# Optimization experiments

Measured on AMD Instinct MI355X. Metric: run time of the kernel, lower is better.

## Reference

```python
import jax, jax.numpy as jnp
import numpy as np
from jax import lax

EPS = 1e-7
N_CLASS = 10
ROUTINGS = 3
DIM_PRIMARY = 8
DIM_DIGIT = 16


def squash(s, axis=-1):
    sq = jnp.sum(jnp.square(s), axis=axis, keepdims=True)
    scale = sq / (1.0 + sq) / jnp.sqrt(sq + EPS)
    return scale * s


def setup_inputs() -> dict:
    key = jax.random.key(0)
    ks = jax.random.split(key, 6)
    B, H, W, C = 16, 100, 64, 1
    x = jax.random.normal(ks[0], (B, H, W, C), dtype=jnp.float32)
    # conv1: 9x9, 1 -> 256, stride 1, valid, relu
    conv1_w = jax.random.normal(ks[1], (9, 9, 1, 256), dtype=jnp.float32) * 0.05
    conv1_b = jnp.zeros((256,), dtype=jnp.float32)
    # PrimaryCap conv: 9x9, 256 -> 32*8=256, stride 2, valid, linear
    pc_w = jax.random.normal(ks[2], (9, 9, 256, 256), dtype=jnp.float32) * 0.02
    pc_b = jnp.zeros((256,), dtype=jnp.float32)
    # primary caps: conv1 out 92x56 -> pc conv out 42x24 -> 42*24*32 = 32256 caps
    n_in_caps = 42 * 24 * 32
    caps_W = jax.random.normal(ks[3], (N_CLASS, n_in_caps, DIM_DIGIT, DIM_PRIMARY), dtype=jnp.float32) * 0.05
    return {"x": x, "conv1_w": conv1_w, "conv1_b": conv1_b, "pc_w": pc_w, "pc_b": pc_b, "caps_W": caps_W}


def reference(x, conv1_w, conv1_b, pc_w, pc_b, caps_W):
    dn = ("NHWC", "HWIO", "NHWC")
    # Conv1 + relu: [B,92,56,256]
    y = lax.conv_general_dilated(x, conv1_w, (1, 1), "VALID", dimension_numbers=dn) + conv1_b
    y = jax.nn.relu(y)
    # PrimaryCap conv (stride 2): [B,42,24,256]
    p = lax.conv_general_dilated(y, pc_w, (2, 2), "VALID", dimension_numbers=dn) + pc_b
    B = p.shape[0]
    # reshape to capsules [B, I, 8] and squash
    u = squash(p.reshape(B, -1, DIM_PRIMARY))
    # predictions u_hat[b,j,i,d] = W[j,i,d,k] u[b,i,k]  -> [B, J, I, 16]
    u_hat = jnp.einsum("bik,jidk->bjid", u, caps_W)
    # dynamic routing
    b = jnp.zeros(u_hat.shape[:3], dtype=u_hat.dtype)  # [B, J, I]
    v = None
    for r in range(ROUTINGS):
        c = jax.nn.softmax(b, axis=1)  # over output capsules J
        s = jnp.einsum("bji,bjid->bjd", c, u_hat)
        v = squash(s)  # [B, J, 16]
        if r < ROUTINGS - 1:
            b = b + jnp.einsum("bjd,bjid->bji", v, u_hat)
    return v
```

## Files before the change

kernel.cpp:

```cpp
#include <hip/hip_runtime.h>
#include <hip/hip_bf16.h>
#include <hip/hip_fp16.h>
#include <stdint.h>

typedef __bf16 bf16x8_t __attribute__((ext_vector_type(8)));
typedef float  f32x4_t  __attribute__((ext_vector_type(4)));

#define PLANE_H (16L * 32256 * 32)
#define PSTRIDE 4128768L

__device__ __forceinline__ void gld_lds16(const void* g, void* l) {
    __builtin_amdgcn_global_load_lds(
        (const __attribute__((address_space(1))) uint32_t*)g,
        (__attribute__((address_space(3))) uint32_t*)l, 16, 0, 0);
}

__global__ __launch_bounds__(256) void k_conv1(
    const float* __restrict__ x, const float* __restrict__ w,
    const float* __restrict__ bias, __hip_bfloat16* __restrict__ y)
{
    const int b  = blockIdx.x / 92;
    const int oh = blockIdx.x % 92;
    const int oc = threadIdx.x;
    float wr[81];
#pragma unroll
    for (int t = 0; t < 81; ++t) wr[t] = w[t * 256 + oc];
    const float bs = bias[oc];
    const float* xb = x + (b * 100 + oh) * 64;
    __hip_bfloat16* yb = y + ((b * 92 + oh) * 56) * 256 + oc;
    for (int owg = 0; owg < 56; owg += 4) {
        float a0 = bs, a1 = bs, a2 = bs, a3 = bs;
#pragma unroll
        for (int kh = 0; kh < 9; ++kh) {
            const float* xr = xb + kh * 64 + owg;
            float xv[12];
#pragma unroll
            for (int t = 0; t < 12; ++t) xv[t] = xr[t];
#pragma unroll
            for (int kw = 0; kw < 9; ++kw) {
                const float wv = wr[kh * 9 + kw];
                a0 = fmaf(xv[kw + 0], wv, a0);
                a1 = fmaf(xv[kw + 1], wv, a1);
                a2 = fmaf(xv[kw + 2], wv, a2);
                a3 = fmaf(xv[kw + 3], wv, a3);
            }
        }
        yb[(owg + 0) * 256] = __float2bfloat16(fmaxf(a0, 0.f));
        yb[(owg + 1) * 256] = __float2bfloat16(fmaxf(a1, 0.f));
        yb[(owg + 2) * 256] = __float2bfloat16(fmaxf(a2, 0.f));
        yb[(owg + 3) * 256] = __float2bfloat16(fmaxf(a3, 0.f));
    }
}

__global__ __launch_bounds__(256) void k_wt(
    const float* __restrict__ w, __hip_bfloat16* __restrict__ wt)
{
    const int idx = blockIdx.x * 256 + threadIdx.x;
    const int oc  = idx / 20736;
    const int k   = idx - oc * 20736;
    wt[idx] = __float2bfloat16(w[k * 256 + oc]);
}

__global__ __launch_bounds__(256, 2) void k_pcconv2(
    const __hip_bfloat16* __restrict__ y,
    const __hip_bfloat16* __restrict__ wt,
    float* __restrict__ pbase)
{
    __shared__ __hip_bfloat16 lA[128 * 32];
    __shared__ __hip_bfloat16 lB[256 * 32];
    const int mbx = (blockIdx.x & 7) * 16 + (blockIdx.x >> 3);
    if (mbx >= 126) return;
    const int z = blockIdx.y;
    float* __restrict__ p = pbase + (long)z * PSTRIDE;

    const int tid  = threadIdx.x;
    const int trow = tid >> 2;
    const int quad = tid & 3;
    const int sq   = quad ^ ((trow >> 1) & 3);

    int ybase[2];
#pragma unroll
    for (int r = 0; r < 2; ++r) {
        const int m  = mbx * 128 + r * 64 + trow;
        const int b  = m / 1008;
        const int rm = m - b * 1008;
        const int oh = rm / 24;
        const int ow = rm - oh * 24;
        ybase[r] = ((b * 92 + 2 * oh) * 56 + 2 * ow) * 256 + sq * 8;
    }
    int wbase[4];
#pragma unroll
    for (int r = 0; r < 4; ++r)
        wbase[r] = (r * 64 + trow) * 20736 + sq * 8;

    f32x4_t acc[4][8];
#pragma unroll
    for (int mi = 0; mi < 4; ++mi)
#pragma unroll
        for (int ni = 0; ni < 8; ++ni)
            acc[mi][ni] = (f32x4_t){0.f, 0.f, 0.f, 0.f};

    const int wv   = tid >> 6;
    const int lane = tid & 63;
    const int mw   = (wv >> 1) * 64;
    const int nwb  = (wv & 1) * 128;
    const int lr   = lane & 15;
    const int lq   = lane >> 4;
    const int koff = (lq ^ ((lr >> 1) & 3)) * 8;

    for (int kc = z * 108; kc < z * 108 + 108; ++kc) {
        const int k0   = kc * 32;
        const int khw  = k0 >> 8;
        const int ic0  = k0 & 255;
        const int kh   = khw / 9;
        const int kw2  = khw - kh * 9;
        const int aoff = (kh * 56 + kw2) * 256 + ic0;
        __syncthreads();
#pragma unroll
        for (int r = 0; r < 2; ++r)
            gld_lds16(y + ybase[r] + aoff, &lA[r * 2048 + tid * 8]);
#pragma unroll
        for (int r = 0; r < 4; ++r)
            gld_lds16(wt + wbase[r] + k0, &lB[r * 2048 + tid * 8]);
        __builtin_amdgcn_s_waitcnt(0);
        __syncthreads();
        bf16x8_t af[4], bfr[8];
#pragma unroll
        for (int mi = 0; mi < 4; ++mi)
            af[mi] = *(const bf16x8_t*)&lA[(mw + mi * 16 + lr) * 32 + koff];
#pragma unroll
        for (int ni = 0; ni < 8; ++ni)
            bfr[ni] = *(const bf16x8_t*)&lB[(nwb + ni * 16 + lr) * 32 + koff];
#pragma unroll
        for (int mi = 0; mi < 4; ++mi)
#pragma unroll
            for (int ni = 0; ni < 8; ++ni)
                acc[mi][ni] = __builtin_amdgcn_mfma_f32_16x16x32_bf16(
                    af[mi], bfr[ni], acc[mi][ni], 0, 0, 0);
    }
#pragma unroll
    for (int mi = 0; mi < 4; ++mi)
#pragma unroll
        for (int ni = 0; ni < 8; ++ni) {
            const int col = nwb + ni * 16 + lr;
#pragma unroll
            for (int rr = 0; rr < 4; ++rr) {
                const int row = mbx * 128 + mw + mi * 16 + lq * 4 + rr;
                p[row * 256 + col] = acc[mi][ni][rr];
            }
        }
}

__global__ __launch_bounds__(256) void k_squash(
    const float* __restrict__ P, const float* __restrict__ bias, float* u)
{
    const int g = blockIdx.x * 256 + threadIdx.x;
    const int base = g * 8;
    const int cb = (g & 31) * 8;
    float v[8];
#pragma unroll
    for (int t = 0; t < 8; ++t) v[t] = bias[cb + t];
#pragma unroll
    for (int z = 0; z < 6; ++z) {
        const float4 a0 = *(const float4*)(P + z * PSTRIDE + base);
        const float4 a1 = *(const float4*)(P + z * PSTRIDE + base + 4);
        v[0] += a0.x; v[1] += a0.y; v[2] += a0.z; v[3] += a0.w;
        v[4] += a1.x; v[5] += a1.y; v[6] += a1.z; v[7] += a1.w;
    }
    float sq = 0.f;
#pragma unroll
    for (int t = 0; t < 8; ++t) sq += v[t] * v[t];
    const float sc = sq / ((1.f + sq) * sqrtf(sq + 1e-7f));
#pragma unroll
    for (int t = 0; t < 8; ++t) u[base + t] = v[t] * sc;
}

__global__ __launch_bounds__(256) void k_uhat2(
    const float* __restrict__ u, const float* __restrict__ W, __half* __restrict__ uh)
{
    __shared__ __half lbuf[8 * 64 * 32];
    const int bh  = blockIdx.x;
    const int ic  = blockIdx.y;
    const int tid = threadIdx.x;
    const int q   = tid & 3;
    const int il  = tid >> 2;
    const int i   = ic * 64 + il;

    for (int jg = 0; jg < 5; ++jg) {
        const float* wb0 = W + ((long)(2 * jg) * 32256 + i) * 128 + q * 32;
        const float* wb1 = wb0 + (long)32256 * 128;
        float4 w0[8], w1[8];
#pragma unroll
        for (int t = 0; t < 8; ++t) w0[t] = *(const float4*)(wb0 + t * 4);
#pragma unroll
        for (int t = 0; t < 8; ++t) w1[t] = *(const float4*)(wb1 + t * 4);
        if (jg) __syncthreads();
#pragma unroll
        for (int b = 0; b < 8; ++b) {
            const float* up = u + ((bh * 8 + b) * 32256 + i) * 8;
            const float4 u0 = *(const float4*)up;
            const float4 u1 = *(const float4*)(up + 4);
            union { __half h[8]; uint4 v; } pk;
#pragma unroll
            for (int d = 0; d < 4; ++d) {
                const float4 a = w0[2 * d], c = w0[2 * d + 1];
                pk.h[d] = __float2half(
                    a.x * u0.x + a.y * u0.y + a.z * u0.z + a.w * u0.w +
                    c.x * u1.x + c.y * u1.y + c.z * u1.z + c.w * u1.w);
            }
#pragma unroll
            for (int d = 0; d < 4; ++d) {
                const float4 a = w1[2 * d], c = w1[2 * d + 1];
                pk.h[4 + d] = __float2half(
                    a.x * u0.x + a.y * u0.y + a.z * u0.z + a.w * u0.w +
                    c.x * u1.x + c.y * u1.y + c.z * u1.z + c.w * u1.w);
            }
            *(uint4*)&lbuf[(b * 64 + il) * 32 + q * 8] = pk.v;
        }
        __syncthreads();
        __half* pb = uh + (long)jg * PLANE_H + ((long)(bh * 8) * 32256 + ic * 64) * 32;
#pragma unroll
        for (int b = 0; b < 8; ++b) {
            const uint4 v = *(const uint4*)&lbuf[b * 2048 + tid * 8];
            *(uint4*)(pb + (long)b * (32256 * 32) + tid * 8) = v;
        }
    }
}

__global__ __launch_bounds__(256) void k_route4(
    const __half* __restrict__ uh, const float* __restrict__ vsum,
    float* __restrict__ sp)
{
    __shared__ float red[4 * 160];
    const int b     = blockIdx.x;
    const int chunk = blockIdx.y;
    const int tid   = threadIdx.x;
    const int lane  = tid & 63;
    const int wv    = tid >> 6;
    const int q     = lane & 3;
    const int ig    = lane >> 2;

    float vs[10][4];
#pragma unroll
    for (int j = 0; j < 10; ++j) {
        const float4 t = *(const float4*)(vsum + (b * 10 + j) * 16 + q * 4);
        vs[j][0] = t.x; vs[j][1] = t.y; vs[j][2] = t.z; vs[j][3] = t.w;
    }
    float acc[10][4];
#pragma unroll
    for (int j = 0; j < 10; ++j)
#pragma unroll
        for (int t = 0; t < 4; ++t) acc[j][t] = 0.f;

    const int ib = chunk * 576 + wv * 16 + ig;
    for (int ps = 0; ps < 9; ++ps) {
        const int i = ib + ps * 64;
        const long rb = ((long)b * 32256 + i) * 32 + q * 8;
        uint4 r[5];
#pragma unroll
        for (int jg = 0; jg < 5; ++jg)
            r[jg] = *(const uint4*)(uh + jg * PLANE_H + rb);
        float uhf[10][4];
#pragma unroll
        for (int jg = 0; jg < 5; ++jg) {
            const unsigned wd[4] = {r[jg].x, r[jg].y, r[jg].z, r[jg].w};
#pragma unroll
            for (int h2 = 0; h2 < 4; ++h2) {
                const __half2 hh = *(const __half2*)&wd[h2];
                const int j  = jg * 2 + (h2 >> 1);
                const int d0 = (h2 & 1) * 2;
                uhf[j][d0 + 0] = __low2float(hh);
                uhf[j][d0 + 1] = __high2float(hh);
            }
        }
        float logit[10];
#pragma unroll
        for (int j = 0; j < 10; ++j) {
            float lg = vs[j][0] * uhf[j][0] + vs[j][1] * uhf[j][1]
                     + vs[j][2] * uhf[j][2] + vs[j][3] * uhf[j][3];
            lg += __shfl_xor(lg, 1);
            lg += __shfl_xor(lg, 2);
            logit[j] = lg;
        }
        float mx = logit[0];
#pragma unroll
        for (int j = 1; j < 10; ++j) mx = fmaxf(mx, logit[j]);
        float den = 0.f, e[10];
#pragma unroll
        for (int j = 0; j < 10; ++j) { e[j] = __expf(logit[j] - mx); den += e[j]; }
        const float inv = __builtin_amdgcn_rcpf(den);
#pragma unroll
        for (int j = 0; j < 10; ++j) {
            const float c = e[j] * inv;
#pragma unroll
            for (int t = 0; t < 4; ++t) acc[j][t] = fmaf(c, uhf[j][t], acc[j][t]);
        }
    }
#pragma unroll
    for (int j = 0; j < 10; ++j)
#pragma unroll
        for (int t = 0; t < 4; ++t) {
            float v2 = acc[j][t];
            v2 += __shfl_xor(v2, 4);
            v2 += __shfl_xor(v2, 8);
            v2 += __shfl_xor(v2, 16);
            v2 += __shfl_xor(v2, 32);
            if (lane < 4) red[wv * 160 + j * 16 + q * 4 + t] = v2;
        }
    __syncthreads();
    if (tid < 160) {
        const float s = red[tid] + red[160 + tid] + red[320 + tid] + red[480 + tid];
        atomicAdd(&sp[b * 160 + tid], s);
    }
}

__global__ void k_finish(const float* __restrict__ sp, float* __restrict__ vsum,
                         float* __restrict__ out, const int fin)
{
    const int t = threadIdx.x;
    if (t >= 160) return;
    const float* s = sp + t * 16;
    float sv[16]; float sq = 0.f;
#pragma unroll
    for (int d = 0; d < 16; ++d) { sv[d] = s[d]; sq += sv[d] * sv[d]; }
    const float sc = sq / ((1.f + sq) * sqrtf(sq + 1e-7f));
    if (fin) {
#pragma unroll
        for (int d = 0; d < 16; ++d) out[t * 16 + d] = sv[d] * sc;
    } else {
        float* vp = vsum + t * 16;
#pragma unroll
        for (int d = 0; d < 16; ++d) vp[d] += sv[d] * sc;
    }
}

extern "C" void kernel_launch(void* const* d_in, const int* in_sizes, int n_in,
                              void* d_out, int out_size, void* d_ws, size_t ws_size,
                              hipStream_t stream)
{
    const float* x   = (const float*)d_in[0];
    const float* c1w = (const float*)d_in[1];
    const float* c1b = (const float*)d_in[2];
    const float* pcw = (const float*)d_in[3];
    const float* pcb = (const float*)d_in[4];
    const float* cW  = (const float*)d_in[5];
    float* out = (float*)d_out;

    char* ws = (char*)d_ws;
    float* P  = (float*)(ws);
    __hip_bfloat16* y  = (__hip_bfloat16*)(ws + 99090432);
    __hip_bfloat16* wt = (__hip_bfloat16*)(ws + 141295616);
    __half* uh = (__half*)(ws + 16515072);
    float* sp   = (float*)(ws + 181665792);
    float* vsum = (float*)(ws + 181696512);

    hipMemsetAsync(sp, 0, (3 * 2560 + 2560) * 4, stream);

    k_conv1<<<16 * 92, 256, 0, stream>>>(x, c1w, c1b, y);
    k_wt<<<20736, 256, 0, stream>>>(pcw, wt);
    k_pcconv2<<<dim3(128, 6), 256, 0, stream>>>(y, wt, P);
    k_squash<<<2016, 256, 0, stream>>>(P, pcb, P);
    k_uhat2<<<dim3(2, 504), 256, 0, stream>>>(P, cW, uh);
    for (int it = 0; it < 3; ++it) {
        k_route4<<<dim3(16, 56), 256, 0, stream>>>(uh, vsum, sp + it * 2560);
        k_finish<<<1, 256, 0, stream>>>(sp + it * 2560, vsum, out, it == 2 ? 1 : 0);
    }
}
```

Measured before the change: 764.6 us.

## Retile primary-cap conv, write fp16 partials, fuse first routing sum into uhat

The PrimaryCap conv GEMM now uses 128x128 tiles with K=64 per stage, split-K 12 ways, and a rotated K start per block. Partial sums are stored in fp16 instead of fp32, which halves partial traffic and lets squash read packed halves. The first routing iteration (uniform coupling 0.1) is fused into k_uhat2 through shuffle reduction and atomics, which removes one k_route4 pass over u_hat. The costs are fp16 rounding of the partial sums and extra atomic and shuffle work inside uhat.

```diff
diff --git a/kernel.cpp b/kernel.cpp
--- a/kernel.cpp
+++ b/kernel.cpp
@@ -6,8 +6,8 @@
 typedef __bf16 bf16x8_t __attribute__((ext_vector_type(8)));
 typedef float  f32x4_t  __attribute__((ext_vector_type(4)));
 
-#define PLANE_H (16L * 32256 * 32)
-#define PSTRIDE 4128768L
+#define PLANE_H   (16L * 32256 * 32)
+#define PSTRIDE_H 4128768L
 
 __device__ __forceinline__ void gld_lds16(const void* g, void* l) {
     __builtin_amdgcn_global_load_lds(
@@ -61,55 +61,58 @@
     wt[idx] = __float2bfloat16(w[k * 256 + oc]);
 }
 
-__global__ __launch_bounds__(256, 2) void k_pcconv2(
+__global__ __launch_bounds__(256, 4) void k_pcconv3(
     const __hip_bfloat16* __restrict__ y,
     const __hip_bfloat16* __restrict__ wt,
-    float* __restrict__ pbase)
-{
-    __shared__ __hip_bfloat16 lA[128 * 32];
-    __shared__ __hip_bfloat16 lB[256 * 32];
-    const int mbx = (blockIdx.x & 7) * 16 + (blockIdx.x >> 3);
+    __half* __restrict__ pbase)
+{
+    __shared__ __hip_bfloat16 lA[128 * 64];
+    __shared__ __hip_bfloat16 lB[128 * 64];
+    const int gx  = blockIdx.x;
+    const int nb  = gx & 1;
+    const int tm  = gx >> 1;
+    const int mbx = (tm & 7) * 16 + (tm >> 3);
     if (mbx >= 126) return;
     const int z = blockIdx.y;
-    float* __restrict__ p = pbase + (long)z * PSTRIDE;
+    __half* __restrict__ p = pbase + (long)z * PSTRIDE_H;
 
     const int tid  = threadIdx.x;
-    const int trow = tid >> 2;
-    const int quad = tid & 3;
-    const int sq   = quad ^ ((trow >> 1) & 3);
-
-    int ybase[2];
-#pragma unroll
-    for (int r = 0; r < 2; ++r) {
-        const int m  = mbx * 128 + r * 64 + trow;
+    const int lane = tid & 63;
+    const int w    = tid >> 6;
+    const int oct  = lane >> 3;
+    const int c    = (lane & 7) ^ oct;
+
+    int ybaseA[4], wbB[4];
+#pragma unroll
+    for (int j = 0; j < 4; ++j) {
+        const int r  = w * 32 + j * 8 + oct;
+        const int m  = mbx * 128 + r;
         const int b  = m / 1008;
         const int rm = m - b * 1008;
         const int oh = rm / 24;
         const int ow = rm - oh * 24;
-        ybase[r] = ((b * 92 + 2 * oh) * 56 + 2 * ow) * 256 + sq * 8;
-    }
-    int wbase[4];
-#pragma unroll
-    for (int r = 0; r < 4; ++r)
-        wbase[r] = (r * 64 + trow) * 20736 + sq * 8;
-
-    f32x4_t acc[4][8];
+        ybaseA[j] = ((b * 92 + 2 * oh) * 56 + 2 * ow) * 256 + c * 8;
+        wbB[j]    = (nb * 128 + r) * 20736 + c * 8;
+    }
+
+    f32x4_t acc[4][4];
 #pragma unroll
     for (int mi = 0; mi < 4; ++mi)
 #pragma unroll
-        for (int ni = 0; ni < 8; ++ni)
+        for (int ni = 0; ni < 4; ++ni)
             acc[mi][ni] = (f32x4_t){0.f, 0.f, 0.f, 0.f};
 
-    const int wv   = tid >> 6;
-    const int lane = tid & 63;
-    const int mw   = (wv >> 1) * 64;
-    const int nwb  = (wv & 1) * 128;
-    const int lr   = lane & 15;
-    const int lq   = lane >> 4;
-    const int koff = (lq ^ ((lr >> 1) & 3)) * 8;
-
-    for (int kc = z * 108; kc < z * 108 + 108; ++kc) {
-        const int k0   = kc * 32;
+    const int mw = (w >> 1) * 64;
+    const int nw = (w & 1) * 64;
+    const int lr = lane & 15;
+    const int lq = lane >> 4;
+    const int koff0 = ((lq + 0) ^ (lr & 7)) * 8;
+    const int koff1 = ((lq + 4) ^ (lr & 7)) * 8;
+
+    const int off = (gx * 11 + z * 5) % 27;
+    for (int it = 0; it < 27; ++it) {
+        const int kc   = z * 27 + ((it + off) % 27);
+        const int k0   = kc * 64;
         const int khw  = k0 >> 8;
         const int ic0  = k0 & 255;
         const int kh   = khw / 9;
@@ -117,55 +120,63 @@
         const int aoff = (kh * 56 + kw2) * 256 + ic0;
         __syncthreads();
 #pragma unroll
-        for (int r = 0; r < 2; ++r)
-            gld_lds16(y + ybase[r] + aoff, &lA[r * 2048 + tid * 8]);
-#pragma unroll
-        for (int r = 0; r < 4; ++r)
-            gld_lds16(wt + wbase[r] + k0, &lB[r * 2048 + tid * 8]);
+        for (int j = 0; j < 4; ++j)
+            gld_lds16(y + ybaseA[j] + aoff, &lA[(w * 32 + j * 8) * 64 + lane * 8]);
+#pragma unroll
+        for (int j = 0; j < 4; ++j)
+            gld_lds16(wt + wbB[j] + k0, &lB[(w * 32 + j * 8) * 64 + lane * 8]);
         __builtin_amdgcn_s_waitcnt(0);
         __syncthreads();
-        bf16x8_t af[4], bfr[8];
-#pragma unroll
-        for (int mi = 0; mi < 4; ++mi)
-            af[mi] = *(const bf16x8_t*)&lA[(mw + mi * 16 + lr) * 32 + koff];
-#pragma unroll
-        for (int ni = 0; ni < 8; ++ni)
-            bfr[ni] = *(const bf16x8_t*)&lB[(nwb + ni * 16 + lr) * 32 + koff];
-#pragma unroll
-        for (int mi = 0; mi < 4; ++mi)
-#pragma unroll
-            for (int ni = 0; ni < 8; ++ni)
-                acc[mi][ni] = __builtin_amdgcn_mfma_f32_16x16x32_bf16(
-                    af[mi], bfr[ni], acc[mi][ni], 0, 0, 0);
+#pragma unroll
+        for (int t = 0; t < 2; ++t) {
+            const int koff = t ? koff1 : koff0;
+            bf16x8_t af[4], bfr[4];
+#pragma unroll
+            for (int mi = 0; mi < 4; ++mi)
+                af[mi] = *(const bf16x8_t*)&lA[(mw + mi * 16 + lr) * 64 + koff];
+#pragma unroll
+            for (int ni = 0; ni < 4; ++ni)
+                bfr[ni] = *(const bf16x8_t*)&lB[(nw + ni * 16 + lr) * 64 + koff];
+#pragma unroll
+            for (int mi = 0; mi < 4; ++mi)
+#pragma unroll
+                for (int ni = 0; ni < 4; ++ni)
+                    acc[mi][ni] = __builtin_amdgcn_mfma_f32_16x16x32_bf16(
+                        af[mi], bfr[ni], acc[mi][ni], 0, 0, 0);
+        }
     }
 #pragma unroll
     for (int mi = 0; mi < 4; ++mi)
 #pragma unroll
-        for (int ni = 0; ni < 8; ++ni) {
-            const int col = nwb + ni * 16 + lr;
+        for (int ni = 0; ni < 4; ++ni) {
+            const int col = nb * 128 + nw + ni * 16 + lr;
 #pragma unroll
             for (int rr = 0; rr < 4; ++rr) {
                 const int row = mbx * 128 + mw + mi * 16 + lq * 4 + rr;
-                p[row * 256 + col] = acc[mi][ni][rr];
+                p[(long)row * 256 + col] = __float2half(acc[mi][ni][rr]);
             }
         }
 }
 
 __global__ __launch_bounds__(256) void k_squash(
-    const float* __restrict__ P, const float* __restrict__ bias, float* u)
+    const __half* __restrict__ Ph, const float* __restrict__ bias, float* __restrict__ u)
 {
     const int g = blockIdx.x * 256 + threadIdx.x;
-    const int base = g * 8;
+    const long base = (long)g * 8;
     const int cb = (g & 31) * 8;
     float v[8];
 #pragma unroll
     for (int t = 0; t < 8; ++t) v[t] = bias[cb + t];
 #pragma unroll
-    for (int z = 0; z < 6; ++z) {
-        const float4 a0 = *(const float4*)(P + z * PSTRIDE + base);
-        const float4 a1 = *(const float4*)(P + z * PSTRIDE + base + 4);
-        v[0] += a0.x; v[1] += a0.y; v[2] += a0.z; v[3] += a0.w;
-        v[4] += a1.x; v[5] += a1.y; v[6] += a1.z; v[7] += a1.w;
+    for (int z = 0; z < 12; ++z) {
+        const uint4 r = *(const uint4*)(Ph + z * PSTRIDE_H + base);
+        const unsigned wd[4] = {r.x, r.y, r.z, r.w};
+#pragma unroll
+        for (int h2 = 0; h2 < 4; ++h2) {
+            const __half2 hh = *(const __half2*)&wd[h2];
+            v[h2 * 2 + 0] += __low2float(hh);
+            v[h2 * 2 + 1] += __high2float(hh);
+        }
     }
     float sq = 0.f;
 #pragma unroll
@@ -176,15 +187,19 @@
 }
 
 __global__ __launch_bounds__(256) void k_uhat2(
-    const float* __restrict__ u, const float* __restrict__ W, __half* __restrict__ uh)
+    const float* __restrict__ u, const float* __restrict__ W, __half* __restrict__ uh,
+    float* __restrict__ sp0)
 {
     __shared__ __half lbuf[8 * 64 * 32];
-    const int bh  = blockIdx.x;
-    const int ic  = blockIdx.y;
-    const int tid = threadIdx.x;
-    const int q   = tid & 3;
-    const int il  = tid >> 2;
-    const int i   = ic * 64 + il;
+    __shared__ float red[4 * 256];
+    const int bh   = blockIdx.x;
+    const int ic   = blockIdx.y;
+    const int tid  = threadIdx.x;
+    const int lane = tid & 63;
+    const int wv   = tid >> 6;
+    const int q    = tid & 3;
+    const int il   = tid >> 2;
+    const int i    = ic * 64 + il;
 
     for (int jg = 0; jg < 5; ++jg) {
         const float* wb0 = W + ((long)(2 * jg) * 32256 + i) * 128 + q * 32;
@@ -203,19 +218,34 @@
             union { __half h[8]; uint4 v; } pk;
 #pragma unroll
             for (int d = 0; d < 4; ++d) {
-                const float4 a = w0[2 * d], c = w0[2 * d + 1];
+                const float4 a = w0[2 * d], cc = w0[2 * d + 1];
                 pk.h[d] = __float2half(
                     a.x * u0.x + a.y * u0.y + a.z * u0.z + a.w * u0.w +
-                    c.x * u1.x + c.y * u1.y + c.z * u1.z + c.w * u1.w);
+                    cc.x * u1.x + cc.y * u1.y + cc.z * u1.z + cc.w * u1.w);
             }
 #pragma unroll
             for (int d = 0; d < 4; ++d) {
-                const float4 a = w1[2 * d], c = w1[2 * d + 1];
+                const float4 a = w1[2 * d], cc = w1[2 * d + 1];
                 pk.h[4 + d] = __float2half(
                     a.x * u0.x + a.y * u0.y + a.z * u0.z + a.w * u0.w +
-                    c.x * u1.x + c.y * u1.y + c.z * u1.z + c.w * u1.w);
+                    cc.x * u1.x + cc.y * u1.y + cc.z * u1.z + cc.w * u1.w);
             }
             *(uint4*)&lbuf[(b * 64 + il) * 32 + q * 8] = pk.v;
+            float rv[8];
+#pragma unroll
+            for (int t = 0; t < 8; ++t) rv[t] = __half2float(pk.h[t]);
+#pragma unroll
+            for (int t = 0; t < 8; ++t) {
+                rv[t] += __shfl_xor(rv[t], 4);
+                rv[t] += __shfl_xor(rv[t], 8);
+                rv[t] += __shfl_xor(rv[t], 16);
+                rv[t] += __shfl_xor(rv[t], 32);
+            }
+            if (lane < 4) {
+#pragma unroll
+                for (int t = 0; t < 8; ++t)
+                    red[wv * 256 + b * 32 + (t >> 2) * 16 + q * 4 + (t & 3)] = rv[t];
+            }
         }
         __syncthreads();
         __half* pb = uh + (long)jg * PLANE_H + ((long)(bh * 8) * 32256 + ic * 64) * 32;
@@ -223,6 +253,11 @@
         for (int b = 0; b < 8; ++b) {
             const uint4 v = *(const uint4*)&lbuf[b * 2048 + tid * 8];
             *(uint4*)(pb + (long)b * (32256 * 32) + tid * 8) = v;
+        }
+        {
+            const float v = red[tid] + red[256 + tid] + red[512 + tid] + red[768 + tid];
+            const int bb = tid >> 5, j2 = (tid >> 4) & 1, dd = tid & 15;
+            atomicAdd(&sp0[((bh * 8 + bb) * 10 + (2 * jg + j2)) * 16 + dd], 0.1f * v);
         }
     }
 }
@@ -347,9 +382,10 @@
     float* out = (float*)d_out;
 
     char* ws = (char*)d_ws;
-    float* P  = (float*)(ws);
-    __hip_bfloat16* y  = (__hip_bfloat16*)(ws + 99090432);
-    __hip_bfloat16* wt = (__hip_bfloat16*)(ws + 141295616);
+    float* u  = (float*)(ws);
+    __half* Ph = (__half*)(ws + 16515072);
+    __hip_bfloat16* y  = (__hip_bfloat16*)(ws + 115605504);
+    __hip_bfloat16* wt = (__hip_bfloat16*)(ws + 157810688);
     __half* uh = (__half*)(ws + 16515072);
     float* sp   = (float*)(ws + 181665792);
     float* vsum = (float*)(ws + 181696512);
@@ -358,11 +394,12 @@
 
     k_conv1<<<16 * 92, 256, 0, stream>>>(x, c1w, c1b, y);
     k_wt<<<20736, 256, 0, stream>>>(pcw, wt);
-    k_pcconv2<<<dim3(128, 6), 256, 0, stream>>>(y, wt, P);
-    k_squash<<<2016, 256, 0, stream>>>(P, pcb, P);
-    k_uhat2<<<dim3(2, 504), 256, 0, stream>>>(P, cW, uh);
-    for (int it = 0; it < 3; ++it) {
-        k_route4<<<dim3(16, 56), 256, 0, stream>>>(uh, vsum, sp + it * 2560);
-        k_finish<<<1, 256, 0, stream>>>(sp + it * 2560, vsum, out, it == 2 ? 1 : 0);
-    }
-}
+    k_pcconv3<<<dim3(256, 12), 256, 0, stream>>>(y, wt, Ph);
+    k_squash<<<2016, 256, 0, stream>>>(Ph, pcb, u);
+    k_uhat2<<<dim3(2, 504), 256, 0, stream>>>(u, cW, uh, sp);
+    k_finish<<<1, 256, 0, stream>>>(sp, vsum, out, 0);
+    k_route4<<<dim3(16, 56), 256, 0, stream>>>(uh, vsum, sp + 2560);
+    k_finish<<<1, 256, 0, stream>>>(sp + 2560, vsum, out, 0);
+    k_route4<<<dim3(16, 56), 256, 0, stream>>>(uh, vsum, sp + 5120);
+    k_finish<<<1, 256, 0, stream>>>(sp + 5120, vsum, out, 1);
+}
```

Result: faster. 709.5 us (-7.2%).
